# Performance work log

Measured on AMD Instinct MI355X. Metric: run time of the kernel, lower is better.

## Reference

```python
import jax, jax.numpy as jnp
import numpy as np

N = 65536
NUM_STATE = 128
NUM_HIDDEN = 256
NUM_EMBED = 128


def setup_inputs() -> dict:
    key = jax.random.key(0)
    ks = jax.random.split(key, 8)
    s1 = jax.random.normal(ks[0], (N, NUM_STATE), dtype=jnp.float32)
    s2 = jax.random.normal(ks[1], (N, NUM_STATE), dtype=jnp.float32)
    # kaiming_normal_(fan_in, linear): std = 1/sqrt(fan_in)
    W1 = jax.random.normal(ks[2], (NUM_HIDDEN, NUM_STATE), dtype=jnp.float32) / np.sqrt(NUM_STATE)
    b1 = jnp.zeros((NUM_HIDDEN,), dtype=jnp.float32)
    W2 = jax.random.normal(ks[3], (NUM_HIDDEN, NUM_HIDDEN), dtype=jnp.float32) / np.sqrt(NUM_HIDDEN)
    b2 = jnp.zeros((NUM_HIDDEN,), dtype=jnp.float32)
    W3 = jax.random.normal(ks[4], (NUM_EMBED, NUM_HIDDEN), dtype=jnp.float32) / np.sqrt(NUM_HIDDEN)
    b3 = jnp.zeros((NUM_EMBED,), dtype=jnp.float32)
    return {"s1": s1, "s2": s2, "W1": W1, "b1": b1, "W2": W2, "b2": b2, "W3": W3, "b3": b3}


def _embed(x, W1, b1, W2, b2, W3, b3):
    h = jax.nn.selu(x @ W1.T + b1)
    h = jax.nn.selu(h @ W2.T + b2)
    return h @ W3.T + b3  # [N, num_embedding]


def reference(s1, s2, W1, b1, W2, b2, W3, b3):
    e1 = _embed(s1, W1, b1, W2, b2, W3, b3)
    e2 = _embed(s2, W1, b1, W2, b2, W3, b3)
    # diag(e1 @ e2.T) == per-row dot product (same math, O(N*d) not O(N^2*d))
    dots = jnp.einsum('nd,nd->n', e1, e2)
    out = dots / (jnp.linalg.norm(e1, axis=1) * jnp.linalg.norm(e2, axis=1))
    out = (out + 1.0) / 2.0
    return jax.nn.sigmoid(out)
```

## Files before the change

### kernel.cpp

```cpp
#include <hip/hip_runtime.h>


typedef __bf16 bf16x8 __attribute__((ext_vector_type(8)));
typedef __bf16 bf16x4 __attribute__((ext_vector_type(4)));
typedef float  f32x4  __attribute__((ext_vector_type(4)));

constexpr int WS_W1 = 0;
constexpr int WS_W2 = 32768;
constexpr int WS_W3 = 98304;

__device__ __forceinline__ float selu_f(float x) {
    const float scale = 1.0507009873554805f;
    const float sa    = 1.7580993408473766f;
    float xp = fmaxf(x, 0.f);
    float xn = fminf(x, 0.f);
    return fmaf(scale, xp, sa * (__expf(xn) - 1.f));
}

template<int COLS>
__device__ __forceinline__ bf16x8 read_act(const __bf16* lds, int row, int kcol) {
    unsigned byte = (unsigned)((row * COLS + kcol) * 2) ^ ((unsigned)(row & 7) << 4);
    return *(const bf16x8*)((const char*)lds + byte);
}

template<bool SELU, int COLS>
__device__ __forceinline__ void store_act(__bf16* lds, int row, int col0, f32x4 a) {
    float v0 = a[0], v1 = a[1], v2 = a[2], v3 = a[3];
    if (SELU) { v0 = selu_f(v0); v1 = selu_f(v1); v2 = selu_f(v2); v3 = selu_f(v3); }
    bf16x4 u;
    u[0] = (__bf16)v0; u[1] = (__bf16)v1; u[2] = (__bf16)v2; u[3] = (__bf16)v3;
    unsigned byte = (unsigned)((row * COLS + col0) * 2) ^ ((unsigned)(row & 7) << 4);
    *(bf16x4*)((char*)lds + byte) = u;
}

__global__ void pack_weights_kernel(const float* __restrict__ W1,
                                    const float* __restrict__ W2,
                                    const float* __restrict__ W3,
                                    __bf16* __restrict__ ws) {
    int t = blockIdx.x * blockDim.x + threadIdx.x;
    const float* W; int K, KS, f, base;
    if (t < 4096)       { W = W1; K = 128; KS = 4; f = t;         base = WS_W1; }
    else if (t < 12288) { W = W2; K = 256; KS = 8; f = t - 4096;  base = WS_W2; }
    else                { W = W3; K = 256; KS = 8; f = t - 12288; base = WS_W3; }
    int lane = f & 63;
    int ks   = (f >> 6) % KS;
    int ct   = f / (64 * KS);
    int row  = ct * 16 + (lane & 15);
    int k0   = ks * 32 + (lane >> 4) * 8;
    const float* src = W + (size_t)row * K + k0;
    __bf16* dst = ws + base + (size_t)f * 8;
#pragma unroll
    for (int j = 0; j < 8; ++j) dst[j] = (__bf16)src[j];
}

__global__ __launch_bounds__(256, 3)
void embed_sim_kernel(const float* __restrict__ s1, const float* __restrict__ s2,
                      const float* __restrict__ b1, const float* __restrict__ b2,
                      const float* __restrict__ b3,
                      const __bf16* __restrict__ wf, float* __restrict__ out) {
    __shared__ __align__(16) __bf16 Xs[64 * 128];
    __shared__ __align__(16) __bf16 hA[64 * 256];

    const int tid  = threadIdx.x;
    const int wave = tid >> 6;
    const int lane = tid & 63;
    const int lr   = lane & 15;
    const int kg   = lane >> 4;
    const int p0   = blockIdx.x * 32;

    __bf16* h2hi = hA;
    float*  red  = (float*)(hA + 64 * 128);

#pragma unroll
    for (int it = 0; it < 4; ++it) {
        int idx = tid + it * 256;
        int row = idx >> 4;
        int k0  = (idx & 15) << 3;
        const float* src = (row < 32) ? (s1 + (size_t)(p0 + row) * 128 + k0)
                                      : (s2 + (size_t)(p0 + row - 32) * 128 + k0);
        float4 v0 = *(const float4*)(src);
        float4 v1 = *(const float4*)(src + 4);
        bf16x8 w;
        w[0] = (__bf16)v0.x; w[1] = (__bf16)v0.y; w[2] = (__bf16)v0.z; w[3] = (__bf16)v0.w;
        w[4] = (__bf16)v1.x; w[5] = (__bf16)v1.y; w[6] = (__bf16)v1.z; w[7] = (__bf16)v1.w;
        unsigned byte = (unsigned)((row * 128 + k0) * 2) ^ ((unsigned)(row & 7) << 4);
        *(bf16x8*)((char*)Xs + byte) = w;
    }
    __syncthreads();

    {
        bf16x8 wfr[4][4]; f32x4 bv[4];
#pragma unroll
        for (int ti = 0; ti < 4; ++ti) {
            int t = wave * 4 + ti;
#pragma unroll
            for (int ks = 0; ks < 4; ++ks)
                wfr[ti][ks] = *(const bf16x8*)(wf + WS_W1 + (size_t)((t * 4 + ks) * 64 + lane) * 8);
            bv[ti] = *(const f32x4*)(b1 + t * 16 + kg * 4);
        }
#pragma unroll
        for (int s = 0; s < 4; ++s) {
            const int row = s * 16 + lr;
            bf16x8 xfr[4];
#pragma unroll
            for (int ks = 0; ks < 4; ++ks) xfr[ks] = read_act<128>(Xs, row, ks * 32 + kg * 8);
#pragma unroll
            for (int ti = 0; ti < 4; ++ti) {
                f32x4 acc = bv[ti];
#pragma unroll
                for (int ks = 0; ks < 4; ++ks)
                    acc = __builtin_amdgcn_mfma_f32_16x16x32_bf16(wfr[ti][ks], xfr[ks], acc, 0, 0, 0);
                store_act<true, 256>(hA, row, (wave * 4 + ti) * 16 + kg * 4, acc);
            }
        }
    }
    __syncthreads();

    {
        f32x4 acc[4][4];
#pragma unroll
        for (int ti = 0; ti < 4; ++ti) {
            f32x4 b = *(const f32x4*)(b2 + (wave * 4 + ti) * 16 + kg * 4);
#pragma unroll
            for (int s = 0; s < 4; ++s) acc[ti][s] = b;
        }
#pragma unroll
        for (int kh = 0; kh < 2; ++kh) {
            bf16x8 wfr[4][4];
#pragma unroll
            for (int ti = 0; ti < 4; ++ti) {
                int t = wave * 4 + ti;
#pragma unroll
                for (int ks = 0; ks < 4; ++ks)
                    wfr[ti][ks] = *(const bf16x8*)(wf + WS_W2 + (size_t)((t * 8 + kh * 4 + ks) * 64 + lane) * 8);
            }
#pragma unroll
            for (int s = 0; s < 4; ++s) {
                const int row = s * 16 + lr;
                bf16x8 hfr[4];
#pragma unroll
                for (int ks = 0; ks < 4; ++ks)
                    hfr[ks] = read_act<256>(hA, row, kh * 128 + ks * 32 + kg * 8);
#pragma unroll
                for (int ti = 0; ti < 4; ++ti)
#pragma unroll
                    for (int ks = 0; ks < 4; ++ks)
                        acc[ti][s] = __builtin_amdgcn_mfma_f32_16x16x32_bf16(
                            wfr[ti][ks], hfr[ks], acc[ti][s], 0, 0, 0);
            }
        }
        if (wave < 2) {
#pragma unroll
            for (int ti = 0; ti < 4; ++ti)
#pragma unroll
                for (int s = 0; s < 4; ++s)
                    store_act<true, 128>(Xs, s * 16 + lr, (wave * 4 + ti) * 16 + kg * 4, acc[ti][s]);
        }
        __syncthreads();
        if (wave >= 2) {
#pragma unroll
            for (int ti = 0; ti < 4; ++ti)
#pragma unroll
                for (int s = 0; s < 4; ++s)
                    store_act<true, 128>(h2hi, s * 16 + lr, ((wave - 2) * 4 + ti) * 16 + kg * 4, acc[ti][s]);
        }
    }
    __syncthreads();

    f32x4 acc3[2][4];
    {
#pragma unroll
        for (int ti = 0; ti < 2; ++ti) {
            f32x4 b = *(const f32x4*)(b3 + (wave * 2 + ti) * 16 + kg * 4);
#pragma unroll
            for (int s = 0; s < 4; ++s) acc3[ti][s] = b;
        }
#pragma unroll
        for (int kh = 0; kh < 2; ++kh) {
            const __bf16* src = (kh == 0) ? Xs : h2hi;
            bf16x8 wfr[2][4];
#pragma unroll
            for (int ti = 0; ti < 2; ++ti) {
                int t = wave * 2 + ti;
#pragma unroll
                for (int ks = 0; ks < 4; ++ks)
                    wfr[ti][ks] = *(const bf16x8*)(wf + WS_W3 + (size_t)((t * 8 + kh * 4 + ks) * 64 + lane) * 8);
            }
#pragma unroll
            for (int s = 0; s < 4; ++s) {
                const int row = s * 16 + lr;
                bf16x8 hfr[4];
#pragma unroll
                for (int ks = 0; ks < 4; ++ks)
                    hfr[ks] = read_act<128>(src, row, ks * 32 + kg * 8);
#pragma unroll
                for (int ti = 0; ti < 2; ++ti)
#pragma unroll
                    for (int ks = 0; ks < 4; ++ks)
                        acc3[ti][s] = __builtin_amdgcn_mfma_f32_16x16x32_bf16(
                            wfr[ti][ks], hfr[ks], acc3[ti][s], 0, 0, 0);
            }
        }
    }

    {
        float d0 = 0.f, a0 = 0.f, c0 = 0.f;
        float d1 = 0.f, a1 = 0.f, c1 = 0.f;
#pragma unroll
        for (int ti = 0; ti < 2; ++ti)
#pragma unroll
            for (int j = 0; j < 4; ++j) {
                float e1a = acc3[ti][0][j], e2a = acc3[ti][2][j];
                float e1b = acc3[ti][1][j], e2b = acc3[ti][3][j];
                d0 = fmaf(e1a, e2a, d0); a0 = fmaf(e1a, e1a, a0); c0 = fmaf(e2a, e2a, c0);
                d1 = fmaf(e1b, e2b, d1); a1 = fmaf(e1b, e1b, a1); c1 = fmaf(e2b, e2b, c1);
            }
#pragma unroll
        for (int off = 16; off < 64; off <<= 1) {
            d0 += __shfl_xor(d0, off); a0 += __shfl_xor(a0, off); c0 += __shfl_xor(c0, off);
            d1 += __shfl_xor(d1, off); a1 += __shfl_xor(a1, off); c1 += __shfl_xor(c1, off);
        }
        if (kg == 0) {
            float* r0 = red + ((wave * 32) + lr) * 3;
            r0[0] = d0; r0[1] = a0; r0[2] = c0;
            float* r1 = red + ((wave * 32) + 16 + lr) * 3;
            r1[0] = d1; r1[1] = a1; r1[2] = c1;
        }
    }
    __syncthreads();

    if (tid < 32) {
        const int p = tid;
        float D = 0.f, A = 0.f, C = 0.f;
#pragma unroll
        for (int w = 0; w < 4; ++w) {
            const float* r = red + ((w * 32) + p) * 3;
            D += r[0]; A += r[1]; C += r[2];
        }
        float r = D * rsqrtf(A * C);
        float x = (r + 1.f) * 0.5f;
        out[p0 + p] = 1.f / (1.f + __expf(-x));
    }
}

extern "C" void kernel_launch(void* const* d_in, const int* in_sizes, int n_in,
                              void* d_out, int out_size, void* d_ws, size_t ws_size,
                              hipStream_t stream) {
    const float* s1 = (const float*)d_in[0];
    const float* s2 = (const float*)d_in[1];
    const float* W1 = (const float*)d_in[2];
    const float* b1 = (const float*)d_in[3];
    const float* W2 = (const float*)d_in[4];
    const float* b2 = (const float*)d_in[5];
    const float* W3 = (const float*)d_in[6];
    const float* b3 = (const float*)d_in[7];
    __bf16* wf = (__bf16*)d_ws;
    float*  outp = (float*)d_out;

    pack_weights_kernel<<<64, 256, 0, stream>>>(W1, W2, W3, wf);

    const int npairs = in_sizes[0] / 128;
    embed_sim_kernel<<<npairs / 32, 256, 0, stream>>>(s1, s2, b1, b2, b3, wf, outp);
}
```

Measured before the change: 57.66 us.

## Load layer-1 inputs directly from global into MFMA fragments, drop Xs LDS buffer

Removes the staging of s1/s2 through an LDS buffer. Each lane now reads its float rows from global memory and converts them to bf16 fragments in registers, which also removes one barrier. Layer-2 output is written back into the single hA buffer after a sync, and the reduction scratch gets its own small array. Cutting LDS from about 48KB to about 34KB per block, together with raising launch bounds to 4 blocks, aims for higher occupancy. The cost is uncoalesced per-lane global reads of 32-byte chunks and more register pressure.

```diff
diff --git a/kernel.cpp b/kernel.cpp
--- a/kernel.cpp
+++ b/kernel.cpp
@@ -17,19 +17,18 @@
     return fmaf(scale, xp, sa * (__expf(xn) - 1.f));
 }
 
-template<int COLS>
 __device__ __forceinline__ bf16x8 read_act(const __bf16* lds, int row, int kcol) {
-    unsigned byte = (unsigned)((row * COLS + kcol) * 2) ^ ((unsigned)(row & 7) << 4);
+    unsigned byte = (unsigned)((row * 256 + kcol) * 2) ^ ((unsigned)(row & 7) << 4);
     return *(const bf16x8*)((const char*)lds + byte);
 }
 
-template<bool SELU, int COLS>
+template<bool SELU>
 __device__ __forceinline__ void store_act(__bf16* lds, int row, int col0, f32x4 a) {
     float v0 = a[0], v1 = a[1], v2 = a[2], v3 = a[3];
     if (SELU) { v0 = selu_f(v0); v1 = selu_f(v1); v2 = selu_f(v2); v3 = selu_f(v3); }
     bf16x4 u;
     u[0] = (__bf16)v0; u[1] = (__bf16)v1; u[2] = (__bf16)v2; u[3] = (__bf16)v3;
-    unsigned byte = (unsigned)((row * COLS + col0) * 2) ^ ((unsigned)(row & 7) << 4);
+    unsigned byte = (unsigned)((row * 256 + col0) * 2) ^ ((unsigned)(row & 7) << 4);
     *(bf16x4*)((char*)lds + byte) = u;
 }
 
@@ -53,13 +52,13 @@
     for (int j = 0; j < 8; ++j) dst[j] = (__bf16)src[j];
 }
 
-__global__ __launch_bounds__(256, 3)
+__global__ __launch_bounds__(256, 4)
 void embed_sim_kernel(const float* __restrict__ s1, const float* __restrict__ s2,
                       const float* __restrict__ b1, const float* __restrict__ b2,
                       const float* __restrict__ b3,
                       const __bf16* __restrict__ wf, float* __restrict__ out) {
-    __shared__ __align__(16) __bf16 Xs[64 * 128];
     __shared__ __align__(16) __bf16 hA[64 * 256];
+    __shared__ __align__(16) float  red[4 * 32 * 3];
 
     const int tid  = threadIdx.x;
     const int wave = tid >> 6;
@@ -68,26 +67,6 @@
     const int kg   = lane >> 4;
     const int p0   = blockIdx.x * 32;
 
-    __bf16* h2hi = hA;
-    float*  red  = (float*)(hA + 64 * 128);
-
-#pragma unroll
-    for (int it = 0; it < 4; ++it) {
-        int idx = tid + it * 256;
-        int row = idx >> 4;
-        int k0  = (idx & 15) << 3;
-        const float* src = (row < 32) ? (s1 + (size_t)(p0 + row) * 128 + k0)
-                                      : (s2 + (size_t)(p0 + row - 32) * 128 + k0);
-        float4 v0 = *(const float4*)(src);
-        float4 v1 = *(const float4*)(src + 4);
-        bf16x8 w;
-        w[0] = (__bf16)v0.x; w[1] = (__bf16)v0.y; w[2] = (__bf16)v0.z; w[3] = (__bf16)v0.w;
-        w[4] = (__bf16)v1.x; w[5] = (__bf16)v1.y; w[6] = (__bf16)v1.z; w[7] = (__bf16)v1.w;
-        unsigned byte = (unsigned)((row * 128 + k0) * 2) ^ ((unsigned)(row & 7) << 4);
-        *(bf16x8*)((char*)Xs + byte) = w;
-    }
-    __syncthreads();
-
     {
         bf16x8 wfr[4][4]; f32x4 bv[4];
 #pragma unroll
@@ -101,16 +80,26 @@
 #pragma unroll
         for (int s = 0; s < 4; ++s) {
             const int row = s * 16 + lr;
+            const float* xr = (row < 32) ? (s1 + (size_t)(p0 + row) * 128)
+                                         : (s2 + (size_t)(p0 + row - 32) * 128);
             bf16x8 xfr[4];
 #pragma unroll
-            for (int ks = 0; ks < 4; ++ks) xfr[ks] = read_act<128>(Xs, row, ks * 32 + kg * 8);
+            for (int ks = 0; ks < 4; ++ks) {
+                const float* p = xr + ks * 32 + kg * 8;
+                float4 v0 = *(const float4*)(p);
+                float4 v1 = *(const float4*)(p + 4);
+                bf16x8 w;
+                w[0] = (__bf16)v0.x; w[1] = (__bf16)v0.y; w[2] = (__bf16)v0.z; w[3] = (__bf16)v0.w;
+                w[4] = (__bf16)v1.x; w[5] = (__bf16)v1.y; w[6] = (__bf16)v1.z; w[7] = (__bf16)v1.w;
+                xfr[ks] = w;
+            }
 #pragma unroll
             for (int ti = 0; ti < 4; ++ti) {
                 f32x4 acc = bv[ti];
 #pragma unroll
                 for (int ks = 0; ks < 4; ++ks)
                     acc = __builtin_amdgcn_mfma_f32_16x16x32_bf16(wfr[ti][ks], xfr[ks], acc, 0, 0, 0);
-                store_act<true, 256>(hA, row, (wave * 4 + ti) * 16 + kg * 4, acc);
+                store_act<true>(hA, row, (wave * 4 + ti) * 16 + kg * 4, acc);
             }
         }
     }
@@ -140,7 +129,7 @@
                 bf16x8 hfr[4];
 #pragma unroll
                 for (int ks = 0; ks < 4; ++ks)
-                    hfr[ks] = read_act<256>(hA, row, kh * 128 + ks * 32 + kg * 8);
+                    hfr[ks] = read_act(hA, row, kh * 128 + ks * 32 + kg * 8);
 #pragma unroll
                 for (int ti = 0; ti < 4; ++ti)
 #pragma unroll
@@ -149,21 +138,12 @@
                             wfr[ti][ks], hfr[ks], acc[ti][s], 0, 0, 0);
             }
         }
-        if (wave < 2) {
-#pragma unroll
-            for (int ti = 0; ti < 4; ++ti)
-#pragma unroll
-                for (int s = 0; s < 4; ++s)
-                    store_act<true, 128>(Xs, s * 16 + lr, (wave * 4 + ti) * 16 + kg * 4, acc[ti][s]);
-        }
         __syncthreads();
-        if (wave >= 2) {
-#pragma unroll
-            for (int ti = 0; ti < 4; ++ti)
-#pragma unroll
-                for (int s = 0; s < 4; ++s)
-                    store_act<true, 128>(h2hi, s * 16 + lr, ((wave - 2) * 4 + ti) * 16 + kg * 4, acc[ti][s]);
-        }
+#pragma unroll
+        for (int ti = 0; ti < 4; ++ti)
+#pragma unroll
+            for (int s = 0; s < 4; ++s)
+                store_act<true>(hA, s * 16 + lr, (wave * 4 + ti) * 16 + kg * 4, acc[ti][s]);
     }
     __syncthreads();
 
@@ -177,7 +157,6 @@
         }
 #pragma unroll
         for (int kh = 0; kh < 2; ++kh) {
-            const __bf16* src = (kh == 0) ? Xs : h2hi;
             bf16x8 wfr[2][4];
 #pragma unroll
             for (int ti = 0; ti < 2; ++ti) {
@@ -192,7 +171,7 @@
                 bf16x8 hfr[4];
 #pragma unroll
                 for (int ks = 0; ks < 4; ++ks)
-                    hfr[ks] = read_act<128>(src, row, ks * 32 + kg * 8);
+                    hfr[ks] = read_act(hA, row, kh * 128 + ks * 32 + kg * 8);
 #pragma unroll
                 for (int ti = 0; ti < 2; ++ti)
 #pragma unroll
```

New measurement: 101.8 us. 76.5% more time.
